# Kernel optimization log

Hardware: AMD Instinct MI355X
Metric: run time of the kernel (lower is better)

Reference implementation:

```python
import jax, jax.numpy as jnp
import numpy as np

N = 6144
D = 128
TAU = 0.1
ADJ_P = 0.005  # edge density


def _l2_normalize(x, eps=1e-12):
    # matches torch F.normalize: x / max(||x||, eps)
    n = jnp.sqrt(jnp.sum(x * x, axis=-1, keepdims=True))
    return x / jnp.maximum(n, eps)


def setup_inputs() -> dict:
    key = jax.random.key(0)
    ks = jax.random.split(key, 8)
    embF = jax.random.normal(ks[0], (N, D), jnp.float32)
    embM = jax.random.normal(ks[1], (N, D), jnp.float32)
    embP = jax.random.normal(ks[2], (N, D), jnp.float32)
    FM_adj = (jax.random.uniform(ks[3], (N, N)) < ADJ_P).astype(jnp.float32)
    FP_adj = (jax.random.uniform(ks[4], (N, N)) < ADJ_P).astype(jnp.float32)
    W1 = jax.random.normal(ks[5], (2 * D, D), jnp.float32) * (1.0 / np.sqrt(2 * D))
    b1 = jnp.zeros((D,), jnp.float32)
    W2 = jax.random.normal(ks[6], (D, 2), jnp.float32) * (1.0 / np.sqrt(D))
    b2 = jnp.zeros((2,), jnp.float32)
    return {"embF": embF, "embM": embM, "embP": embP,
            "FM_adj": FM_adj, "FP_adj": FP_adj,
            "W1": W1, "b1": b1, "W2": W2, "b2": b2}


def reference(embF, embM, embP, FM_adj, FP_adj, W1, b1, W2, b2):
    # attention-weighted neighbor aggregation
    FM_repr = (FM_adj @ embM) / jnp.maximum(FM_adj.sum(1, keepdims=True), 1.0)
    FP_repr = (FP_adj @ embP) / jnp.maximum(FP_adj.sum(1, keepdims=True), 1.0)
    # stack(dim=1).view(N,-1) == concat along feature dim
    feat = jnp.concatenate([FM_repr, FP_repr], axis=1)            # [N, 2D]
    h = jnp.maximum(feat @ W1 + b1, 0.0)                           # ReLU (dropout inactive in eval)
    weights = jax.nn.softmax(h @ W2 + b2, axis=-1)                 # [N, 2]

    Fn = _l2_normalize(embF)
    Mn = _l2_normalize(embM)
    Pn = _l2_normalize(embP)

    FM_sim = jnp.exp((Fn @ Mn.T) / TAU)                            # [N, Nm]
    FP_sim = jnp.exp((Fn @ Pn.T) / TAU)                            # [N, Np]

    FM_pos = jnp.sum(FM_sim * FM_adj, axis=1)
    FP_pos = jnp.sum(FP_sim * FP_adj, axis=1)
    FM_neg = jnp.sum(FM_sim, axis=1) - FM_pos
    FP_neg = jnp.sum(FP_sim, axis=1) - FP_pos

    w0, w1w = weights[:, 0], weights[:, 1]
    wp = w0 * FM_pos + w1w * FP_pos
    wn = w0 * FM_neg + w1w * FP_neg

    nei_count = jnp.maximum(FM_adj.sum(1) + FP_adj.sum(1), 1.0)
    ratio = wp / (wp + wn) / nei_count
    ratio = jnp.maximum(ratio, 1e-10)
    loss = jnp.mean(-jnp.log(ratio))
    return loss, weights
```

## Files before the change

### kernel.cpp

```cpp
#include <hip/hip_runtime.h>
#include <hip/hip_bf16.h>

#define NN 6144
#define DD 128
#define PBL 136
#define INV_TAU 10.0f

typedef __attribute__((ext_vector_type(4))) float f32x4;
typedef __attribute__((ext_vector_type(8))) short s16x8;

__device__ __forceinline__ void ld4_async(const float4* p, float4& d) {
    asm volatile("global_load_dwordx4 %0, %1, off" : "=v"(d) : "v"(p));
}
__device__ __forceinline__ void vm_wait0() {
    asm volatile("s_waitcnt vmcnt(0)" ::: "memory");
}

__global__ void k_normalize(const float* __restrict__ embF,
                            const float* __restrict__ embM,
                            const float* __restrict__ embP,
                            float* __restrict__ Fn,
                            float* __restrict__ rnM, float* __restrict__ rnP,
                            __hip_bfloat16* __restrict__ Fnb,
                            __hip_bfloat16* __restrict__ Mnb,
                            __hip_bfloat16* __restrict__ Pnb) {
    int which = blockIdx.y;
    const float* src = which == 0 ? embF : (which == 1 ? embM : embP);
    __hip_bfloat16* dstb = which == 0 ? Fnb : (which == 1 ? Mnb : Pnb);
    int wave = threadIdx.x >> 6, lane = threadIdx.x & 63;
    int row = blockIdx.x * 4 + wave;
    float2 v = reinterpret_cast<const float2*>(src + (size_t)row * DD)[lane];
    float s = v.x * v.x + v.y * v.y;
#pragma unroll
    for (int m = 1; m <= 32; m <<= 1) s += __shfl_xor(s, m);
    float inv = 1.0f / fmaxf(sqrtf(s), 1e-12f);
    float2 o; o.x = v.x * inv; o.y = v.y * inv;
    if (which == 0)
        reinterpret_cast<float2*>(Fn + (size_t)row * DD)[lane] = o;
    if (lane == 0) {
        if (which == 1) rnM[row] = inv;
        if (which == 2) rnP[row] = inv;
    }
    __hip_bfloat162 ob;
    ob.x = __float2bfloat16(o.x);
    ob.y = __float2bfloat16(o.y);
    reinterpret_cast<__hip_bfloat162*>(dstb + (size_t)row * DD)[lane] = ob;
}

__global__ void k_prep(const float* __restrict__ W1,
                       __hip_bfloat16* __restrict__ W1tb) {
    int n = blockIdx.x, c = threadIdx.x;
    W1tb[n * 256 + c] = __float2bfloat16(W1[c * DD + n]);
}

__device__ __forceinline__ void sparse_body(
        int unit, char* smem,
        const float* __restrict__ FM_adj, const float* __restrict__ FP_adj,
        const float* __restrict__ embM, const float* __restrict__ embP,
        const float* __restrict__ Fn,
        const float* __restrict__ rnM, const float* __restrict__ rnP,
        __hip_bfloat16* __restrict__ featb,
        float* __restrict__ FMpos, float* __restrict__ FPpos,
        float* __restrict__ cntF, float* __restrict__ cntP) {
    float* FnS = (float*)smem;
    int (*lbufT)[5] = (int(*)[5])(smem + 512);
    int* listS = (int*)(smem + 512 + 5120);
    float (*reprS)[DD] = (float(*)[DD])(smem + 512 + 5120 + 512);
    float* posS = (float*)(smem + 512 + 5120 + 512 + 4096);
    int* wvS = (int*)(smem + 512 + 5120 + 512 + 4096 + 32);
    int* Ktot = (int*)(smem + 512 + 5120 + 512 + 4096 + 32 + 16);

    const int row = unit >> 1, h = unit & 1;
    const float* adj  = h ? FP_adj : FM_adj;
    const float* embX = h ? embP : embM;
    const float* RN   = h ? rnP : rnM;
    const int tid = threadIdx.x, wv = tid >> 6, lane = tid & 63;

    if (tid < 32)
        reinterpret_cast<float4*>(FnS)[tid] =
            reinterpret_cast<const float4*>(Fn + (size_t)row * DD)[tid];

    const float4* rp = reinterpret_cast<const float4*>(adj + (size_t)row * NN);
    float4 v0, v1, v2, v3, v4, v5;
    ld4_async(rp + tid,        v0);
    ld4_async(rp + 256 + tid,  v1);
    ld4_async(rp + 512 + tid,  v2);
    ld4_async(rp + 768 + tid,  v3);
    ld4_async(rp + 1024 + tid, v4);
    ld4_async(rp + 1280 + tid, v5);
    vm_wait0();
    float4 vv[6] = {v0, v1, v2, v3, v4, v5};
    int mycnt = 0;
#pragma unroll
    for (int u = 0; u < 6; ++u) {
        int cb = (u * 256 + tid) * 4;
        if (vv[u].x != 0.f) { if (mycnt < 4) lbufT[tid][mycnt] = cb;     mycnt++; }
        if (vv[u].y != 0.f) { if (mycnt < 4) lbufT[tid][mycnt] = cb + 1; mycnt++; }
        if (vv[u].z != 0.f) { if (mycnt < 4) lbufT[tid][mycnt] = cb + 2; mycnt++; }
        if (vv[u].w != 0.f) { if (mycnt < 4) lbufT[tid][mycnt] = cb + 3; mycnt++; }
    }
    int cnt = mycnt < 4 ? mycnt : 4;
    int x = cnt;
#pragma unroll
    for (int d = 1; d < 64; d <<= 1) {
        int y = __shfl_up(x, d);
        if (lane >= d) x += y;
    }
    int t = mycnt;
#pragma unroll
    for (int msk = 1; msk <= 32; msk <<= 1) t += __shfl_xor(t, msk);
    if (tid == 0) Ktot[1] = 0;
    if (lane == 63) wvS[wv] = x;
    __syncthreads();
    if (lane == 0) atomicAdd(&Ktot[1], t);
    if (tid == 0) {
        int s = 0;
#pragma unroll
        for (int i = 0; i < 4; ++i) { int v = wvS[i]; wvS[i] = s; s += v; }
        Ktot[0] = s < 128 ? s : 128;
    }
    __syncthreads();
    int off = wvS[wv] + (x - cnt);
    for (int i = 0; i < cnt; ++i) {
        int s = off + i;
        if (s < 128) listS[s] = lbufT[tid][i];
    }
    __syncthreads();
    const int K = Ktot[0];
    const float trueK = (float)Ktot[1];

    const int hw = tid >> 5, sl = tid & 31;
    float4 f4 = reinterpret_cast<const float4*>(FnS)[sl];
    float4 racc = {0.f, 0.f, 0.f, 0.f};
    float wsum = 0.f;
    for (int k = hw; k < K; k += 8) {
        int j = listS[k];
        float rn = RN[j];
        float4 e = reinterpret_cast<const float4*>(embX + (size_t)j * DD)[sl];
        racc.x += e.x; racc.y += e.y; racc.z += e.z; racc.w += e.w;
        float d = f4.x * e.x + f4.y * e.y + f4.z * e.z + f4.w * e.w;
#pragma unroll
        for (int msk = 1; msk <= 16; msk <<= 1) d += __shfl_xor(d, msk);
        wsum += __expf(d * rn * INV_TAU);
    }
    reinterpret_cast<float4*>(&reprS[hw][0])[sl] = racc;
    if (sl == 0) posS[hw] = wsum;
    __syncthreads();
    if (tid < DD) {
        float s = 0.f;
#pragma unroll
        for (int i = 0; i < 8; ++i) s += reprS[i][tid];
        featb[(size_t)row * (2 * DD) + h * DD + tid] =
            __float2bfloat16(s / fmaxf(trueK, 1.0f));
    }
    if (tid == 0) {
        float p = 0.f;
#pragma unroll
        for (int i = 0; i < 8; ++i) p += posS[i];
        (h ? FPpos : FMpos)[row] = p;
        (h ? cntP : cntF)[row] = trueK;
    }
}

__device__ __forceinline__ void dense_body(
        int unit, char* smem,
        const __hip_bfloat16* __restrict__ Fnb,
        const __hip_bfloat16* __restrict__ Mnb,
        const __hip_bfloat16* __restrict__ Pnb,
        float* __restrict__ FMtot, float* __restrict__ FPtot) {
    __hip_bfloat16 (*Bs)[PBL] = (__hip_bfloat16(*)[PBL])smem;
    const int bx = unit % 48, by = (unit / 48) % 16, half = unit / 768;
    const __hip_bfloat16* Bnb = half ? Pnb : Mnb;
    float* TOT = half ? FPtot : FMtot;
    const int tid = threadIdx.x;
    const int w = tid >> 6, lane = tid & 63;
    const int m = lane & 15, q = lane >> 4;
    const int rb = bx * 128 + w * 32;
    const int j0 = by * (NN / 16);

    s16x8 a[2][4];
#pragma unroll
    for (int g = 0; g < 2; ++g)
#pragma unroll
        for (int ks = 0; ks < 4; ++ks)
            a[g][ks] = *reinterpret_cast<const s16x8*>(
                Fnb + (size_t)(rb + g * 16 + m) * DD + ks * 32 + q * 8);

    float4 s0, s1, s2, s3;
    auto issue = [&](int jc) {
        const float4* gp = reinterpret_cast<const float4*>(Bnb + (size_t)jc * DD);
        ld4_async(gp + tid,       s0);
        ld4_async(gp + 256 + tid, s1);
        ld4_async(gp + 512 + tid, s2);
        ld4_async(gp + 768 + tid, s3);
    };
    auto stash = [&](int idx, const float4& v) {
        *reinterpret_cast<float4*>(&Bs[idx >> 4][(idx & 15) * 8]) = v;
    };

    issue(j0);
    float tot[2][4] = {{0.f, 0.f, 0.f, 0.f}, {0.f, 0.f, 0.f, 0.f}};
    for (int it = 0; it < 6; ++it) {
        vm_wait0();
        __syncthreads();
        stash(tid, s0);
        stash(256 + tid, s1);
        stash(512 + tid, s2);
        stash(768 + tid, s3);
        __syncthreads();
        if (it + 1 < 6) issue(j0 + (it + 1) * 64);
#pragma unroll
        for (int t = 0; t < 4; ++t) {
            s16x8 b[4];
#pragma unroll
            for (int ks = 0; ks < 4; ++ks)
                b[ks] = *reinterpret_cast<const s16x8*>(
                    &Bs[t * 16 + m][ks * 32 + q * 8]);
#pragma unroll
            for (int g = 0; g < 2; ++g) {
                f32x4 acc = {0.f, 0.f, 0.f, 0.f};
#pragma unroll
                for (int ks = 0; ks < 4; ++ks)
                    acc = __builtin_amdgcn_mfma_f32_16x16x32_bf16(
                        a[g][ks], b[ks], acc, 0, 0, 0);
#pragma unroll
                for (int r = 0; r < 4; ++r)
                    tot[g][r] += __expf(acc[r] * INV_TAU);
            }
        }
    }
#pragma unroll
    for (int msk = 1; msk <= 8; msk <<= 1)
#pragma unroll
        for (int g = 0; g < 2; ++g)
#pragma unroll
            for (int r = 0; r < 4; ++r)
                tot[g][r] += __shfl_xor(tot[g][r], msk);
    if (m == 0)
#pragma unroll
        for (int g = 0; g < 2; ++g)
#pragma unroll
            for (int r = 0; r < 4; ++r)
                atomicAdd(&TOT[rb + g * 16 + q * 4 + r], tot[g][r]);
}

__global__ __launch_bounds__(256) void k_main(
        const float* __restrict__ FM_adj, const float* __restrict__ FP_adj,
        const float* __restrict__ embM, const float* __restrict__ embP,
        const float* __restrict__ Fn,
        const float* __restrict__ rnM, const float* __restrict__ rnP,
        const __hip_bfloat16* __restrict__ Fnb,
        const __hip_bfloat16* __restrict__ Mnb,
        const __hip_bfloat16* __restrict__ Pnb,
        __hip_bfloat16* __restrict__ featb,
        float* __restrict__ FMpos, float* __restrict__ FPpos,
        float* __restrict__ FMtot, float* __restrict__ FPtot,
        float* __restrict__ cntF, float* __restrict__ cntP) {
    __shared__ char smem[64 * PBL * 2];
    const int b = blockIdx.x;
    const int u = b / 9, r = b - u * 9;
    if (r == 8)
        dense_body(u, smem, Fnb, Mnb, Pnb, FMtot, FPtot);
    else
        sparse_body(u * 8 + r, smem, FM_adj, FP_adj, embM, embP,
                    Fn, rnM, rnP, featb, FMpos, FPpos, cntF, cntP);
}

__global__ __launch_bounds__(256) void k_mlp2(
        const __hip_bfloat16* __restrict__ featb,
        const __hip_bfloat16* __restrict__ W1tb,
        const float* __restrict__ b1, const float* __restrict__ W2,
        float* __restrict__ z) {
    const int tid = threadIdx.x, w = tid >> 6, lane = tid & 63;
    const int m = lane & 15, q = lane >> 4;
    const int unit = blockIdx.x * 4 + w;
    const int rb = (unit >> 3) * 16, n0 = (unit & 7) * 16;
    f32x4 acc = {0.f, 0.f, 0.f, 0.f};
#pragma unroll
    for (int ks = 0; ks < 8; ++ks) {
        s16x8 a = *reinterpret_cast<const s16x8*>(
            featb + (size_t)(rb + m) * 256 + ks * 32 + q * 8);
        s16x8 b = *reinterpret_cast<const s16x8*>(
            W1tb + (size_t)(n0 + m) * 256 + ks * 32 + q * 8);
        acc = __builtin_amdgcn_mfma_f32_16x16x32_bf16(a, b, acc, 0, 0, 0);
    }
    const int n = n0 + m;
    float bias = b1[n], w20 = W2[2 * n], w21 = W2[2 * n + 1];
#pragma unroll
    for (int r = 0; r < 4; ++r) {
        float h = fmaxf(acc[r] + bias, 0.f);
        float p0 = h * w20, p1 = h * w21;
#pragma unroll
        for (int msk = 1; msk <= 8; msk <<= 1) {
            p0 += __shfl_xor(p0, msk);
            p1 += __shfl_xor(p1, msk);
        }
        if (m == 0) {
            int row = rb + q * 4 + r;
            atomicAdd(&z[2 * row], p0);
            atomicAdd(&z[2 * row + 1], p1);
        }
    }
}

__global__ void k_loss(const float* __restrict__ z, const float* __restrict__ b2,
                       const float* __restrict__ FMpos, const float* __restrict__ FPpos,
                       const float* __restrict__ FMtot, const float* __restrict__ FPtot,
                       const float* __restrict__ cntF, const float* __restrict__ cntP,
                       float* __restrict__ out) {
    __shared__ float red[4];
    const int tid = threadIdx.x;
    const int lane = tid & 63, wv = tid >> 6;
    const int row = blockIdx.x * 256 + tid;
    float z0 = z[row * 2] + b2[0], z1 = z[row * 2 + 1] + b2[1];
    float mx = fmaxf(z0, z1);
    float e0 = expf(z0 - mx), e1 = expf(z1 - mx);
    float inv = 1.0f / (e0 + e1);
    float w0 = e0 * inv, w1 = e1 * inv;
    out[1 + row * 2 + 0] = w0;
    out[1 + row * 2 + 1] = w1;
    float wp = w0 * FMpos[row] + w1 * FPpos[row];
    float wn = w0 * (FMtot[row] - FMpos[row]) + w1 * (FPtot[row] - FPpos[row]);
    float nei = fmaxf(cntF[row] + cntP[row], 1.0f);
    float ratio = wp / (wp + wn) / nei;
    ratio = fmaxf(ratio, 1e-10f);
    float term = -logf(ratio);
#pragma unroll
    for (int msk = 1; msk <= 32; msk <<= 1) term += __shfl_xor(term, msk);
    if (lane == 0) red[wv] = term;
    __syncthreads();
    if (tid == 0)
        atomicAdd(out, (red[0] + red[1] + red[2] + red[3]) * (1.0f / NN));
}

extern "C" void kernel_launch(void* const* d_in, const int* in_sizes, int n_in,
                              void* d_out, int out_size, void* d_ws, size_t ws_size,
                              hipStream_t stream) {
    const float* embF   = (const float*)d_in[0];
    const float* embM   = (const float*)d_in[1];
    const float* embP   = (const float*)d_in[2];
    const float* FM_adj = (const float*)d_in[3];
    const float* FP_adj = (const float*)d_in[4];
    const float* W1     = (const float*)d_in[5];
    const float* b1     = (const float*)d_in[6];
    const float* W2     = (const float*)d_in[7];
    const float* b2     = (const float*)d_in[8];
    float* out = (float*)d_out;

    float* ws = (float*)d_ws;
    float* FMtot = ws;
    float* FPtot = FMtot + NN;
    float* zbuf  = FPtot + NN;
    float* FMpos = zbuf + 2 * NN;
    float* FPpos = FMpos + NN;
    float* cntF  = FPpos + NN;
    float* cntP  = cntF + NN;
    float* rnM   = cntP + NN;
    float* rnP   = rnM + NN;
    float* Fn    = rnP + NN;
    __hip_bfloat16* Fnb = (__hip_bfloat16*)(Fn + (size_t)NN * DD);
    __hip_bfloat16* Mnb = Fnb + (size_t)NN * DD;
    __hip_bfloat16* Pnb = Mnb + (size_t)NN * DD;
    __hip_bfloat16* featb = Pnb + (size_t)NN * DD;
    __hip_bfloat16* W1tb  = featb + (size_t)NN * 256;

    hipMemsetAsync(FMtot, 0, 4 * NN * sizeof(float), stream);
    hipMemsetAsync(d_out, 0, sizeof(float), stream);

    k_normalize<<<dim3(NN / 4, 3), 256, 0, stream>>>(embF, embM, embP,
                                                     Fn, rnM, rnP,
                                                     Fnb, Mnb, Pnb);
    k_prep<<<dim3(128), 256, 0, stream>>>(W1, W1tb);
    k_main<<<dim3(13824), 256, 0, stream>>>(FM_adj, FP_adj, embM, embP,
                                            Fn, rnM, rnP, Fnb, Mnb, Pnb,
                                            featb, FMpos, FPpos, FMtot, FPtot,
                                            cntF, cntP);
    k_mlp2<<<dim3(768), 256, 0, stream>>>(featb, W1tb, b1, W2, zbuf);
    k_loss<<<dim3(NN / 256), 256, 0, stream>>>(zbuf, b2, FMpos, FPpos,
                                               FMtot, FPtot, cntF, cntP, out);
}
```

Measured before the change: 369.4 us.

## Split adjacency nonzero scan into separate kernel before fused gather/dense pass

Moves the dense adjacency-row scan out of the fused sparse/dense kernel into a dedicated k_scan3 kernel. It builds per-row nonzero column lists with global atomics, capped at 64 entries. The gather blocks in k_main then read the compact lists instead of streaming each 24KB adjacency row. This removes the scan and scan-sync work from the blocks interleaved with the MFMA dense tiles. The cost is an extra launch and memset, serialized streaming of the adjacency matrices, and unordered column lists, so summation order is nondeterministic.

```diff
diff --git a/kernel.cpp b/kernel.cpp
--- a/kernel.cpp
+++ b/kernel.cpp
@@ -53,81 +53,61 @@
     W1tb[n * 256 + c] = __float2bfloat16(W1[c * DD + n]);
 }
 
-__device__ __forceinline__ void sparse_body(
+__global__ __launch_bounds__(256) void k_scan3(
+        const float* __restrict__ FM_adj, const float* __restrict__ FP_adj,
+        int* __restrict__ nzbuf, int* __restrict__ nzcnt) {
+    const int h = blockIdx.y;
+    const float* adj = h ? FP_adj : FM_adj;
+    const int row0 = blockIdx.x * 4;
+    const float4* base = reinterpret_cast<const float4*>(adj) + (size_t)row0 * 1536;
+    const int tid = threadIdx.x;
+    int* cntb = nzcnt + h * NN;
+    int* nzb = nzbuf + ((size_t)h * NN) * 64;
+#pragma unroll 4
+    for (int i = 0; i < 24; ++i) {
+        int fi = i * 256 + tid;
+        float4 v = base[fi];
+        int r = (int)(((unsigned)fi * 2731u) >> 22);
+        int row = row0 + r;
+        int col0 = (fi - r * 1536) * 4;
+        float vals[4] = {v.x, v.y, v.z, v.w};
+#pragma unroll
+        for (int c = 0; c < 4; ++c) {
+            if (vals[c] != 0.0f) {
+                int slot = atomicAdd(&cntb[row], 1);
+                if (slot < 64) nzb[(size_t)row * 64 + slot] = col0 + c;
+            }
+        }
+    }
+}
+
+__device__ __forceinline__ void gather_body(
         int unit, char* smem,
-        const float* __restrict__ FM_adj, const float* __restrict__ FP_adj,
         const float* __restrict__ embM, const float* __restrict__ embP,
         const float* __restrict__ Fn,
         const float* __restrict__ rnM, const float* __restrict__ rnP,
+        const int* __restrict__ nzbuf, const int* __restrict__ nzcnt,
         __hip_bfloat16* __restrict__ featb,
         float* __restrict__ FMpos, float* __restrict__ FPpos,
         float* __restrict__ cntF, float* __restrict__ cntP) {
     float* FnS = (float*)smem;
-    int (*lbufT)[5] = (int(*)[5])(smem + 512);
-    int* listS = (int*)(smem + 512 + 5120);
-    float (*reprS)[DD] = (float(*)[DD])(smem + 512 + 5120 + 512);
-    float* posS = (float*)(smem + 512 + 5120 + 512 + 4096);
-    int* wvS = (int*)(smem + 512 + 5120 + 512 + 4096 + 32);
-    int* Ktot = (int*)(smem + 512 + 5120 + 512 + 4096 + 32 + 16);
+    int* listS = (int*)(smem + 512);
+    float (*reprS)[DD] = (float(*)[DD])(smem + 768);
+    float* posS = (float*)(smem + 768 + 4096);
 
     const int row = unit >> 1, h = unit & 1;
-    const float* adj  = h ? FP_adj : FM_adj;
     const float* embX = h ? embP : embM;
     const float* RN   = h ? rnP : rnM;
-    const int tid = threadIdx.x, wv = tid >> 6, lane = tid & 63;
+    const int tid = threadIdx.x;
 
     if (tid < 32)
         reinterpret_cast<float4*>(FnS)[tid] =
             reinterpret_cast<const float4*>(Fn + (size_t)row * DD)[tid];
-
-    const float4* rp = reinterpret_cast<const float4*>(adj + (size_t)row * NN);
-    float4 v0, v1, v2, v3, v4, v5;
-    ld4_async(rp + tid,        v0);
-    ld4_async(rp + 256 + tid,  v1);
-    ld4_async(rp + 512 + tid,  v2);
-    ld4_async(rp + 768 + tid,  v3);
-    ld4_async(rp + 1024 + tid, v4);
-    ld4_async(rp + 1280 + tid, v5);
-    vm_wait0();
-    float4 vv[6] = {v0, v1, v2, v3, v4, v5};
-    int mycnt = 0;
-#pragma unroll
-    for (int u = 0; u < 6; ++u) {
-        int cb = (u * 256 + tid) * 4;
-        if (vv[u].x != 0.f) { if (mycnt < 4) lbufT[tid][mycnt] = cb;     mycnt++; }
-        if (vv[u].y != 0.f) { if (mycnt < 4) lbufT[tid][mycnt] = cb + 1; mycnt++; }
-        if (vv[u].z != 0.f) { if (mycnt < 4) lbufT[tid][mycnt] = cb + 2; mycnt++; }
-        if (vv[u].w != 0.f) { if (mycnt < 4) lbufT[tid][mycnt] = cb + 3; mycnt++; }
-    }
-    int cnt = mycnt < 4 ? mycnt : 4;
-    int x = cnt;
-#pragma unroll
-    for (int d = 1; d < 64; d <<= 1) {
-        int y = __shfl_up(x, d);
-        if (lane >= d) x += y;
-    }
-    int t = mycnt;
-#pragma unroll
-    for (int msk = 1; msk <= 32; msk <<= 1) t += __shfl_xor(t, msk);
-    if (tid == 0) Ktot[1] = 0;
-    if (lane == 63) wvS[wv] = x;
+    const int Ktrue = nzcnt[h * NN + row];
+    const int K = Ktrue < 64 ? Ktrue : 64;
+    if (tid < K)
+        listS[tid] = nzbuf[((size_t)(h * NN + row)) * 64 + tid];
     __syncthreads();
-    if (lane == 0) atomicAdd(&Ktot[1], t);
-    if (tid == 0) {
-        int s = 0;
-#pragma unroll
-        for (int i = 0; i < 4; ++i) { int v = wvS[i]; wvS[i] = s; s += v; }
-        Ktot[0] = s < 128 ? s : 128;
-    }
-    __syncthreads();
-    int off = wvS[wv] + (x - cnt);
-    for (int i = 0; i < cnt; ++i) {
-        int s = off + i;
-        if (s < 128) listS[s] = lbufT[tid][i];
-    }
-    __syncthreads();
-    const int K = Ktot[0];
-    const float trueK = (float)Ktot[1];
 
     const int hw = tid >> 5, sl = tid & 31;
     float4 f4 = reinterpret_cast<const float4*>(FnS)[sl];
@@ -151,14 +131,14 @@
 #pragma unroll
         for (int i = 0; i < 8; ++i) s += reprS[i][tid];
         featb[(size_t)row * (2 * DD) + h * DD + tid] =
-            __float2bfloat16(s / fmaxf(trueK, 1.0f));
+            __float2bfloat16(s / fmaxf((float)Ktrue, 1.0f));
     }
     if (tid == 0) {
         float p = 0.f;
 #pragma unroll
         for (int i = 0; i < 8; ++i) p += posS[i];
         (h ? FPpos : FMpos)[row] = p;
-        (h ? cntP : cntF)[row] = trueK;
+        (h ? cntP : cntF)[row] = (float)Ktrue;
     }
 }
 
@@ -245,10 +225,10 @@
 }
 
 __global__ __launch_bounds__(256) void k_main(
-        const float* __restrict__ FM_adj, const float* __restrict__ FP_adj,
         const float* __restrict__ embM, const float* __restrict__ embP,
         const float* __restrict__ Fn,
         const float* __restrict__ rnM, const float* __restrict__ rnP,
+        const int* __restrict__ nzbuf, const int* __restrict__ nzcnt,
         const __hip_bfloat16* __restrict__ Fnb,
         const __hip_bfloat16* __restrict__ Mnb,
         const __hip_bfloat16* __restrict__ Pnb,
@@ -262,8 +242,8 @@
     if (r == 8)
         dense_body(u, smem, Fnb, Mnb, Pnb, FMtot, FPtot);
     else
-        sparse_body(u * 8 + r, smem, FM_adj, FP_adj, embM, embP,
-                    Fn, rnM, rnP, featb, FMpos, FPpos, cntF, cntP);
+        gather_body(u * 8 + r, smem, embM, embP, Fn, rnM, rnP,
+                    nzbuf, nzcnt, featb, FMpos, FPpos, cntF, cntP);
 }
 
 __global__ __launch_bounds__(256) void k_mlp2(
@@ -363,16 +343,20 @@
     __hip_bfloat16* Pnb = Mnb + (size_t)NN * DD;
     __hip_bfloat16* featb = Pnb + (size_t)NN * DD;
     __hip_bfloat16* W1tb  = featb + (size_t)NN * 256;
+    int* nzbuf = (int*)(W1tb + 128 * 256);
+    int* nzcnt = nzbuf + 2 * (size_t)NN * 64;
 
     hipMemsetAsync(FMtot, 0, 4 * NN * sizeof(float), stream);
+    hipMemsetAsync(nzcnt, 0, 2 * NN * sizeof(int), stream);
     hipMemsetAsync(d_out, 0, sizeof(float), stream);
 
     k_normalize<<<dim3(NN / 4, 3), 256, 0, stream>>>(embF, embM, embP,
                                                      Fn, rnM, rnP,
                                                      Fnb, Mnb, Pnb);
     k_prep<<<dim3(128), 256, 0, stream>>>(W1, W1tb);
-    k_main<<<dim3(13824), 256, 0, stream>>>(FM_adj, FP_adj, embM, embP,
-                                            Fn, rnM, rnP, Fnb, Mnb, Pnb,
+    k_scan3<<<dim3(NN / 4, 2), 256, 0, stream>>>(FM_adj, FP_adj, nzbuf, nzcnt);
+    k_main<<<dim3(13824), 256, 0, stream>>>(embM, embP, Fn, rnM, rnP,
+                                            nzbuf, nzcnt, Fnb, Mnb, Pnb,
                                             featb, FMpos, FPpos, FMtot, FPtot,
                                             cntF, cntP);
     k_mlp2<<<dim3(768), 256, 0, stream>>>(featb, W1tb, b1, W2, zbuf);
```

Result: slower. 445.1 us (+20.5%).
